# Performance work log

Hardware: AMD Instinct MI355X
Metric: run time of the kernel (lower is better)

Reference implementation:

```python
import jax, jax.numpy as jnp
import numpy as np

N, D = 100000, 32      # rows / columns of dist & angle
H, W = 100000, 32      # rows / columns of index matrices
NUM_CLASSES = 22       # size of the eye() one-hot table


def setup_inputs() -> dict:
    key = jax.random.key(0)
    k1, k2, k3, k4, k5 = jax.random.split(key, 5)
    dist = jax.random.uniform(k1, (N, D), dtype=jnp.float32)
    angle = jax.random.uniform(k2, (N, D), dtype=jnp.float32)
    idx_t = jax.random.randint(k3, (H, W), 0, NUM_CLASSES, dtype=jnp.int32)
    index_t = jax.random.randint(k4, (H, W), 0, D + 1, dtype=jnp.int32)
    index_h = jax.random.randint(k5, (H,), 0, N, dtype=jnp.int32)
    return {"dist": dist, "angle": angle, "idx_t": idx_t,
            "index_t": index_t, "index_h": index_h}


def reference(dist, angle, idx_t, index_t, index_h):
    n = dist.shape[0]
    # append a zero column so index D acts as a padding sentinel
    zcol = jnp.zeros((n, 1), dtype=dist.dtype)
    dist_new = jnp.concatenate([dist, zcol], axis=1)    # [N, D+1]
    angle_new = jnp.concatenate([angle, zcol], axis=1)  # [N, D+1]

    h, w = idx_t.shape
    # torch builds ab = index_h @ ones(1, w); equivalent to a broadcast
    ab = jnp.broadcast_to(index_h[:, None], (h, w))     # [h, w]

    dist_t = dist_new[ab, index_t]    # [h, w] gather
    angle_t = angle_new[ab, index_t]  # [h, w] gather

    # eye(22)[idx_t] one-hot lookup, flattened per row -> [h, 22*w]
    x1 = jax.nn.one_hot(idx_t, NUM_CLASSES, dtype=dist.dtype).reshape(h, -1)

    # global min-max normalize of the gathered distances
    dmin = dist_t.min()
    dmax = dist_t.max()
    dist_n = (dist_t - dmin) / (dmax - dmin)

    # [h, 22*w + w + w]
    return jnp.concatenate([x1, dist_n, angle_t], axis=1)
```

## Files before the change

### kernel.cpp

```cpp
#include <hip/hip_runtime.h>

#define DCOLS 32
#define WCOLS 32
#define NUM_CLASSES 22
#define ONEHOT_COLS (NUM_CLASSES * WCOLS)
#define OUT_COLS (ONEHOT_COLS + WCOLS + WCOLS)
#define ROWS_PER_BLOCK 8

typedef float vfloat4 __attribute__((ext_vector_type(4)));


__global__ __launch_bounds__(256) void minmax_kernel(
    const float* __restrict__ dist,
    const int*   __restrict__ index_t,
    const int*   __restrict__ index_h,
    unsigned*    __restrict__ ws,
    int total4)
{
    float vmin = __int_as_float(0x7f800000);
    float vmax = 0.0f;
    const int stride = gridDim.x * blockDim.x;
    for (int i4 = blockIdx.x * blockDim.x + threadIdx.x; i4 < total4; i4 += stride) {
        const int4 it = reinterpret_cast<const int4*>(index_t)[i4];
        const int  h  = i4 >> 3;
        const int  row = index_h[h] * DCOLS;
        float v0 = 0.0f, v1 = 0.0f, v2 = 0.0f, v3 = 0.0f;
        if (it.x < DCOLS) v0 = dist[row + it.x];
        if (it.y < DCOLS) v1 = dist[row + it.y];
        if (it.z < DCOLS) v2 = dist[row + it.z];
        if (it.w < DCOLS) v3 = dist[row + it.w];
        vmin = fminf(fminf(fminf(vmin, v0), fminf(v1, v2)), v3);
        vmax = fmaxf(fmaxf(fmaxf(vmax, v0), fmaxf(v1, v2)), v3);
    }
    #pragma unroll
    for (int off = 32; off > 0; off >>= 1) {
        vmin = fminf(vmin, __shfl_down(vmin, off, 64));
        vmax = fmaxf(vmax, __shfl_down(vmax, off, 64));
    }
    __shared__ float smin[4], smax[4];
    const int lane = threadIdx.x & 63;
    const int wave = threadIdx.x >> 6;
    if (lane == 0) { smin[wave] = vmin; smax[wave] = vmax; }
    __syncthreads();
    if (threadIdx.x == 0) {
        float m = smin[0], M = smax[0];
        #pragma unroll
        for (int k = 1; k < 4; ++k) { m = fminf(m, smin[k]); M = fmaxf(M, smax[k]); }
        atomicMin(ws,             __float_as_uint(-m));
        atomicMax((int*)(ws + 1), __float_as_int(M));
    }
}

__global__ __launch_bounds__(256) void fill_kernel(
    const float* __restrict__ dist,
    const float* __restrict__ angle,
    const int*   __restrict__ idx_t,
    const int*   __restrict__ index_t,
    const int*   __restrict__ index_h,
    const unsigned* __restrict__ ws,
    float*       __restrict__ out,
    int H)
{
    const int h0  = blockIdx.x * ROWS_PER_BLOCK;
    const int tid = threadIdx.x;

    __shared__ int   s_idx[ROWS_PER_BLOCK][WCOLS];
    __shared__ float s_dist[ROWS_PER_BLOCK][WCOLS];
    __shared__ float s_angle[ROWS_PER_BLOCK][WCOLS];

    {
        const float dmin = -__uint_as_float(ws[0]);
        const float dmax =  __uint_as_float(ws[1]);
        const float inv  = 1.0f / (dmax - dmin);
        const int r = tid >> 5;
        const int c = tid & 31;
        const int h = h0 + r;
        if (h < H) {
            const int it = index_t[h * WCOLS + c];
            s_idx[r][c] = idx_t[h * WCOLS + c];
            float dv = 0.0f, av = 0.0f;
            if (it < DCOLS) {
                const int base = index_h[h] * DCOLS;
                dv = dist[base + it];
                av = angle[base + it];
            }
            s_dist[r][c]  = (dv - dmin) * inv;
            s_angle[r][c] = av;
        }
    }
    __syncthreads();

    const bool full = (h0 + ROWS_PER_BLOCK) <= H;
    #pragma unroll
    for (int m = 0; m < 6; ++m) {
        const int t    = m * 256 + tid;
        const int row  = t / 192;
        const int col4 = t - row * 192;
        const int j0   = col4 * 4;
        vfloat4 v4;
        #pragma unroll
        for (int k = 0; k < 4; ++k) {
            const int j = j0 + k;
            float v;
            if (j < ONEHOT_COLS) {
                const int w = j / NUM_CLASSES;
                const int c = j - w * NUM_CLASSES;
                v = (s_idx[row][w] == c) ? 1.0f : 0.0f;
            } else if (j < ONEHOT_COLS + WCOLS) {
                v = s_dist[row][j - ONEHOT_COLS];
            } else {
                v = s_angle[row][j - (ONEHOT_COLS + WCOLS)];
            }
            v4[k] = v;
        }
        if (full) {
            vfloat4* o = reinterpret_cast<vfloat4*>(out + (size_t)h0 * OUT_COLS);
            o[t] = v4;
        } else if (h0 + row < H) {
            vfloat4* o = reinterpret_cast<vfloat4*>(out + (size_t)(h0 + row) * OUT_COLS);
            o[col4] = v4;
        }
    }
}

extern "C" void kernel_launch(void* const* d_in, const int* in_sizes, int n_in,
                              void* d_out, int out_size, void* d_ws, size_t ws_size,
                              hipStream_t stream) {
    const float* dist    = (const float*)d_in[0];
    const float* angle   = (const float*)d_in[1];
    const int*   idx_t   = (const int*)d_in[2];
    const int*   index_t = (const int*)d_in[3];
    const int*   index_h = (const int*)d_in[4];
    float*       out     = (float*)d_out;
    unsigned*    ws      = (unsigned*)d_ws;

    const int H      = in_sizes[4];
    const int total4 = (H * WCOLS) / 4;

    (void)hipMemsetAsync(ws, 0xFF, 8, stream);

    hipLaunchKernelGGL(minmax_kernel, dim3(1024), dim3(256), 0, stream,
                       dist, index_t, index_h, ws, total4);

    const int fill_blocks = (H + ROWS_PER_BLOCK - 1) / ROWS_PER_BLOCK;
    hipLaunchKernelGGL(fill_kernel, dim3(fill_blocks), dim3(256), 0, stream,
                       dist, angle, idx_t, index_t, index_h, ws, out, H);
}
```

Measured before the change: 378.8 us.

## Assign one wavefront per output row using shuffles instead of shared memory

The fill kernel now maps each 64-lane wavefront to a single output row. Row data is exchanged through wave shuffles, so the shared-memory staging arrays and the block-wide barrier are gone. Each lane loads one idx/index value, and the gathered dist/angle values are split across the two half-waves. The cost is extra shuffle instructions per output element, and the number of blocks doubles because each block now covers 4 rows instead of 8.

New measurement: 388.8 us. 2.6% more time.

```diff
diff --git a/kernel.cpp b/kernel.cpp
--- a/kernel.cpp
+++ b/kernel.cpp
@@ -5,7 +5,6 @@
 #define NUM_CLASSES 22
 #define ONEHOT_COLS (NUM_CLASSES * WCOLS)
 #define OUT_COLS (ONEHOT_COLS + WCOLS + WCOLS)
-#define ROWS_PER_BLOCK 8
 
 typedef float vfloat4 __attribute__((ext_vector_type(4)));
 
@@ -61,65 +60,60 @@
     float*       __restrict__ out,
     int H)
 {
-    const int h0  = blockIdx.x * ROWS_PER_BLOCK;
-    const int tid = threadIdx.x;
+    const int wave = threadIdx.x >> 6;
+    const int lane = threadIdx.x & 63;
+    const int h    = blockIdx.x * 4 + wave;
+    if (h >= H) return;
 
-    __shared__ int   s_idx[ROWS_PER_BLOCK][WCOLS];
-    __shared__ float s_dist[ROWS_PER_BLOCK][WCOLS];
-    __shared__ float s_angle[ROWS_PER_BLOCK][WCOLS];
+    const float dmin = -__uint_as_float(ws[0]);
+    const float dmax =  __uint_as_float(ws[1]);
+    const float inv  = 1.0f / (dmax - dmin);
 
-    {
-        const float dmin = -__uint_as_float(ws[0]);
-        const float dmax =  __uint_as_float(ws[1]);
-        const float inv  = 1.0f / (dmax - dmin);
-        const int r = tid >> 5;
-        const int c = tid & 31;
-        const int h = h0 + r;
-        if (h < H) {
-            const int it = index_t[h * WCOLS + c];
-            s_idx[r][c] = idx_t[h * WCOLS + c];
-            float dv = 0.0f, av = 0.0f;
-            if (it < DCOLS) {
-                const int base = index_h[h] * DCOLS;
-                dv = dist[base + it];
-                av = angle[base + it];
-            }
-            s_dist[r][c]  = (dv - dmin) * inv;
-            s_angle[r][c] = av;
-        }
+    const int c    = lane & 31;
+    const int idxv = idx_t[h * WCOLS + c];
+    const int it   = index_t[h * WCOLS + c];
+    const int base = index_h[h] * DCOLS;
+
+    float g = 0.0f;
+    if (lane < 32) {
+        if (it < DCOLS) g = dist[base + it];
+        g = (g - dmin) * inv;
+    } else {
+        if (it < DCOLS) g = angle[base + it];
     }
-    __syncthreads();
 
-    const bool full = (h0 + ROWS_PER_BLOCK) <= H;
+    float* orow = out + (size_t)h * OUT_COLS;
+
     #pragma unroll
-    for (int m = 0; m < 6; ++m) {
-        const int t    = m * 256 + tid;
-        const int row  = t / 192;
-        const int col4 = t - row * 192;
-        const int j0   = col4 * 4;
+    for (int s = 0; s < 2; ++s) {
         vfloat4 v4;
         #pragma unroll
         for (int k = 0; k < 4; ++k) {
-            const int j = j0 + k;
-            float v;
-            if (j < ONEHOT_COLS) {
-                const int w = j / NUM_CLASSES;
-                const int c = j - w * NUM_CLASSES;
-                v = (s_idx[row][w] == c) ? 1.0f : 0.0f;
-            } else if (j < ONEHOT_COLS + WCOLS) {
-                v = s_dist[row][j - ONEHOT_COLS];
-            } else {
-                v = s_angle[row][j - (ONEHOT_COLS + WCOLS)];
-            }
-            v4[k] = v;
+            const int j  = s * 256 + lane * 4 + k;
+            const int w  = j / NUM_CLASSES;
+            const int cc = j - w * NUM_CLASSES;
+            v4[k] = (__shfl(idxv, w, 64) == cc) ? 1.0f : 0.0f;
         }
-        if (full) {
-            vfloat4* o = reinterpret_cast<vfloat4*>(out + (size_t)h0 * OUT_COLS);
-            o[t] = v4;
-        } else if (h0 + row < H) {
-            vfloat4* o = reinterpret_cast<vfloat4*>(out + (size_t)(h0 + row) * OUT_COLS);
-            o[col4] = v4;
+        *reinterpret_cast<vfloat4*>(orow + s * 256 + lane * 4) = v4;
+    }
+
+    {
+        vfloat4 v4;
+        #pragma unroll
+        for (int k = 0; k < 4; ++k) {
+            const int  j    = 512 + lane * 4 + k;
+            const bool isOH = (j < ONEHOT_COLS);
+            const int  w    = isOH ? (j / NUM_CLASSES) : 0;
+            const int  cc   = j - w * NUM_CLASSES;
+            const int  gsrc = isOH ? 0
+                             : (j < ONEHOT_COLS + WCOLS)
+                                 ? (j - ONEHOT_COLS)
+                                 : (j - (ONEHOT_COLS + WCOLS) + 32);
+            const int   ohv = __shfl(idxv, w, 64);
+            const float gv  = __shfl(g, gsrc, 64);
+            v4[k] = isOH ? ((ohv == cc) ? 1.0f : 0.0f) : gv;
         }
+        *reinterpret_cast<vfloat4*>(orow + 512 + lane * 4) = v4;
     }
 }
 
@@ -142,7 +136,7 @@
     hipLaunchKernelGGL(minmax_kernel, dim3(1024), dim3(256), 0, stream,
                        dist, index_t, index_h, ws, total4);
 
-    const int fill_blocks = (H + ROWS_PER_BLOCK - 1) / ROWS_PER_BLOCK;
+    const int fill_blocks = (H + 3) / 4;
     hipLaunchKernelGGL(fill_kernel, dim3(fill_blocks), dim3(256), 0, stream,
                        dist, angle, idx_t, index_t, index_h, ws, out, H);
 }
```
